# Kernel tuning notes

Hardware: AMD Instinct MI355X
Metric: run time of the kernel (lower is better)

The kernel has to match this reference:

```python
import jax, jax.numpy as jnp
import numpy as np

GRID = 28
P = GRID * GRID  # 784 grid points
BY = 1.0 / 13.5  # grid spacing from DTMWeightWrapperLayer(by=1/13.5)
_c = BY * np.stack(np.meshgrid(np.arange(GRID), np.arange(GRID), indexing='ij'), -1).reshape(P, 2).astype(np.float32)
_D2np = ((_c[:, None, :] - _c[None, :, :]) ** 2).sum(-1)
_ORDERnp = np.argsort(_D2np, axis=1)  # per-grid-point neighbor order (constant)
D2S = jnp.asarray(np.take_along_axis(_D2np, _ORDERnp, axis=1), dtype=jnp.float32)  # [P,P] sorted sq dists
ORDER = jnp.asarray(_ORDERnp, dtype=jnp.int32)
TSEQ_A = jnp.asarray(np.linspace(0.06, 0.3, 25), dtype=jnp.float32); KK_A = (0, 1)
TSEQ_B = jnp.asarray(np.linspace(0.14, 0.4, 27), dtype=jnp.float32); KK_B = (0, 1, 2)

def _conv(x, k):
    return jax.lax.conv_general_dilated(x, k, (1, 1), 'SAME', dimension_numbers=('NHWC', 'HWIO', 'NHWC'))

def _dtm(w, m0):
    # distance-to-measure: w [B,P] nonneg weights on the 28x28 grid -> dtm values [B,P]
    ws = w[:, ORDER]                      # [B,P,P] weights ordered by distance from each grid point
    cum = jnp.cumsum(ws, axis=-1)
    m0W = m0 * jnp.sum(w, axis=-1)[:, None, None]  # mass threshold per sample
    eff = jnp.clip(m0W - (cum - ws), 0.0, ws)      # effective weight used from each neighbor
    return jnp.sqrt(jnp.sum(eff * D2S[None], axis=-1) / m0W[:, :, 0])

def _topo(f, tseq, kk, W, b):
    # persistence-landscape features: lambda_k(t) = k-th largest tent value over grid points
    tmax = tseq[-1]
    tent = jnp.maximum(0.0, jnp.minimum(tseq[None, :, None] - f[:, None, :], (tmax - tseq)[None, :, None]))  # [B,T,P]
    top, _ = jax.lax.top_k(tent, max(kk) + 1)       # [B,T,kmax]
    lam = top[..., jnp.asarray(kk)]                 # [B,T,|KK|]
    return lam.reshape(f.shape[0], -1) @ W + b

def setup_inputs() -> dict:
    key = jax.random.key(0)
    ks = jax.random.split(key, 16)
    r = lambda i, s: (0.05 * jax.random.normal(ks[i], s)).astype(jnp.float32)
    z = lambda n: jnp.zeros((n,), jnp.float32)
    return {
        'x': jax.random.uniform(ks[0], (16, 28, 28, 1), jnp.float32),
        'k11': r(1, (3, 3, 1, 32)), 'cb11': z(32), 'k12': r(2, (3, 3, 32, 1)), 'cb12': z(1),
        'k31': r(3, (3, 3, 1, 32)), 'cb31': z(32), 'k32': r(4, (3, 3, 32, 1)), 'cb32': z(1),
        'k41': r(5, (3, 3, 1, 32)), 'cb41': z(32), 'k42': r(6, (3, 3, 32, 1)), 'cb42': z(1),
        'W33': r(7, (50, 16)), 'b33': z(16), 'W43': r(8, (81, 16)), 'b43': z(16),
        'W5': r(9, (50, 16)), 'b5': z(16), 'W6': r(10, (81, 16)), 'b6': z(16),
        'W7': r(11, (848, 64)), 'b7': z(64), 'W8': r(12, (64, 10)), 'b8': z(10),
    }

def reference(x, k11, cb11, k12, cb12, k31, cb31, k32, cb32, k41, cb41, k42, cb42,
              W33, b33, W43, b43, W5, b5, W6, b6, W7, b7, W8, b8):
    relu = jax.nn.relu
    B = 16
    # CNN branch on raw image
    x1 = relu(_conv(relu(_conv(x, k11) + cb11), k12) + cb12).reshape(B, P)
    # DTM functions on the grid
    x2 = x.reshape(B, P)
    x2_1 = _dtm(x2, 0.05)
    x2_2 = _dtm(x2, 0.2)
    # CNN on DTM(m0=0.05) then topo layer
    x3 = relu(_conv(relu(_conv(x2_1.reshape(B, GRID, GRID, 1), k31) + cb31), k32) + cb32).reshape(B, P)
    x3 = relu(_topo(x3, TSEQ_A, KK_A, W33, b33))
    # CNN on DTM(m0=0.2) then topo layer
    x4 = relu(_conv(relu(_conv(x2_2.reshape(B, GRID, GRID, 1), k41) + cb41), k42) + cb42).reshape(B, P)
    x4 = relu(_topo(x4, TSEQ_B, KK_B, W43, b43))
    # topo layers directly on DTM functions
    x5 = relu(_topo(x2_1, TSEQ_A, KK_A, W5, b5))
    x6 = relu(_topo(x2_2, TSEQ_B, KK_B, W6, b6))
    xc = jnp.concatenate((x1, x3, x4, x5, x6), axis=-1)  # [16,848]
    return relu(xc @ W7 + b7) @ W8 + b8  # [16,10]
```

## Files before the change

kernel.cpp:

```cpp
#include <hip/hip_runtime.h>
#include <math.h>

#define GRID 28
#define NP 784

struct PairTab { unsigned int pk[NP]; float d2[NP]; };
constexpr PairTab make_pairs() {
    PairTab t{};
    int cnt[1459] = {};
    for (int di = 0; di < GRID; ++di)
        for (int dj = 0; dj < GRID; ++dj) cnt[di*di + dj*dj]++;
    int off[1459] = {};
    int acc = 0;
    for (int s = 0; s < 1459; ++s) { off[s] = acc; acc += cnt[s]; }
    const double BY2 = (1.0/13.5) * (1.0/13.5);
    for (int di = 0; di < GRID; ++di)
        for (int dj = 0; dj < GRID; ++dj) {
            int s = di*di + dj*dj;
            int o = off[s]++;
            t.pk[o] = (unsigned)((di << 8) | dj);
            t.d2[o] = (float)((double)s * BY2);
        }
    return t;
}
__constant__ PairTab d_PT = make_pairs();

#define CB_SMEM 7328
__device__ void conv_band(const float* __restrict__ in,
                          const float* __restrict__ kA, const float* __restrict__ cbA,
                          const float* __restrict__ kB, const float* __restrict__ cbB,
                          float* __restrict__ outImg, int r0, float* smem)
{
    float* inl = smem;
    float* kAl = inl + 240;
    float* kBl = kAl + 288;
    float* cbl = kBl + 288;
    float* h   = cbl + 32;
    const int tid = threadIdx.x;
    const float cbB0 = cbB[0];

    if (tid < 288)      { kAl[tid] = kA[tid]; kBl[tid] = kB[tid]; }
    else if (tid < 320) cbl[tid - 288] = cbA[tid - 288];
    else if (tid < 560) {
        const int i = tid - 320;
        const int lr = i / 30, col = i % 30;
        const int y = r0 - 2 + lr, ix = col - 1;
        inl[i] = ((unsigned)y < GRID && (unsigned)ix < GRID) ? in[y*GRID + ix] : 0.f;
    }
    {
        float4* h4 = (float4*)h;
        for (int i = tid; i < 6480/4; i += 1024) h4[i] = make_float4(0.f,0.f,0.f,0.f);
    }
    __syncthreads();

    if (tid < 896) {
        const int c = tid & 31, xx = tid >> 5;
        float ka0 = kAl[0*32+c], ka1 = kAl[1*32+c], ka2 = kAl[2*32+c];
        float ka3 = kAl[3*32+c], ka4 = kAl[4*32+c], ka5 = kAl[5*32+c];
        float ka6 = kAl[6*32+c], ka7 = kAl[7*32+c], ka8 = kAl[8*32+c];
        const float bias = cbl[c];
        float w00 = inl[0*30+xx], w01 = inl[0*30+xx+1], w02 = inl[0*30+xx+2];
        float w10 = inl[1*30+xx], w11 = inl[1*30+xx+1], w12 = inl[1*30+xx+2];
        float w20 = inl[2*30+xx], w21 = inl[2*30+xx+1], w22 = inl[2*30+xx+2];
        #pragma unroll
        for (int s = 0; s < 6; ++s) {
            const int y = r0 - 1 + s;
            float a = bias;
            a = fmaf(w00, ka0, a); a = fmaf(w01, ka1, a); a = fmaf(w02, ka2, a);
            a = fmaf(w10, ka3, a); a = fmaf(w11, ka4, a); a = fmaf(w12, ka5, a);
            a = fmaf(w20, ka6, a); a = fmaf(w21, ka7, a); a = fmaf(w22, ka8, a);
            if ((unsigned)y < GRID) h[(s*30 + xx + 1)*36 + c] = fmaxf(a, 0.f);
            if (s < 5) {
                w00 = w10; w01 = w11; w02 = w12;
                w10 = w20; w11 = w21; w12 = w22;
                w20 = inl[(s+3)*30+xx]; w21 = inl[(s+3)*30+xx+1]; w22 = inl[(s+3)*30+xx+2];
            }
        }
    }
    __syncthreads();

    if (tid < 448) {
        const int part = tid & 3, o = tid >> 2;
        const int xx = o % 28, ly = o / 28;
        const int y = r0 + ly;
        float a = 0.f;
        #pragma unroll
        for (int dy = 0; dy < 3; ++dy) {
            #pragma unroll
            for (int dx = 0; dx < 3; ++dx) {
                const float4* hb = (const float4*)&h[((ly+dy)*30 + xx+dx)*36 + part*8];
                const float4* kb = (const float4*)&kBl[(dy*3+dx)*32 + part*8];
                const float4 h0 = hb[0], h1 = hb[1];
                const float4 k0 = kb[0], k1 = kb[1];
                a += h0.x*k0.x; a += h0.y*k0.y; a += h0.z*k0.z; a += h0.w*k0.w;
                a += h1.x*k1.x; a += h1.y*k1.y; a += h1.z*k1.z; a += h1.w*k1.w;
            }
        }
        a += __shfl_xor(a, 1, 64);
        a += __shfl_xor(a, 2, 64);
        if (part == 0) outImg[y*GRID + xx] = fmaxf(a + cbB0, 0.f);
    }
}

__global__ __launch_bounds__(1024, 8) void k1_kernel(const float* __restrict__ x,
        const float* __restrict__ k11, const float* __restrict__ cb11,
        const float* __restrict__ k12, const float* __restrict__ cb12,
        float* __restrict__ ws)
{
    __shared__ float smem[CB_SMEM];
    const int blk = blockIdx.x;
    const int tid = threadIdx.x;

    if (blk < 112) {
        const int img = blk / 7, band = blk % 7;
        conv_band(x + img*NP, k11, cb11, k12, cb12, ws + 25088 + img*NP, band*4, smem);
        return;
    }

    float* wimg = smem;
    float* red  = smem + 784;
    float* out1 = ws;
    float* out2 = ws + 12544;
    const int dblk = blk - 112;
    const int img = dblk / 49, grp = dblk % 49;
    const int w = tid >> 6, lane = tid & 63;

    float v = 0.f;
    if (tid < NP) { v = x[img*NP + tid]; wimg[tid] = v; }
    for (int off = 32; off; off >>= 1) v += __shfl_down(v, off, 64);
    if (lane == 0) red[w] = v;
    __syncthreads();
    float sumw = 0.f;
    #pragma unroll
    for (int i = 0; i < 16; ++i) sumw += red[i];

    const int pix = grp*16 + w;
    const int pr = pix / GRID, pc = pix % GRID;
    const float m0W1 = 0.05f * sumw;
    const float m0W2 = 0.2f  * sumw;
    float a1 = 0.f, a2 = 0.f, carry = 0.f;

    for (int k0 = 0; k0 < NP; k0 += 64) {
        const int idx = k0 + lane;
        const int ii  = idx < NP ? idx : NP-1;
        const unsigned p = d_PT.pk[ii];
        const float dd   = d_PT.d2[ii];
        const int di = (int)(p >> 8);
        const int dj = (int)(p & 255u);
        const int dG = di * GRID;
        const bool rpOK = (pr + di) < GRID;
        const bool rmOK = pr >= di;
        const bool cpOK = (pc + dj) < GRID;
        const bool cmOK = pc >= dj;
        float Wg = 0.f;
        if (rpOK && cpOK)               Wg += wimg[pix + dG + dj];
        if (dj && rpOK && cmOK)         Wg += wimg[pix + dG - dj];
        if (di && rmOK && cpOK)         Wg += wimg[pix - dG + dj];
        if (di && dj && rmOK && cmOK)   Wg += wimg[pix - dG - dj];
        if (idx >= NP) Wg = 0.f;
        float incl = Wg;
        #pragma unroll
        for (int d = 1; d < 64; d <<= 1) {
            const float t = __shfl_up(incl, d, 64);
            if (lane >= d) incl += t;
        }
        const float cumb = carry + (incl - Wg);
        const float e1 = fminf(fmaxf(m0W1 - cumb, 0.f), Wg);
        const float e2 = fminf(fmaxf(m0W2 - cumb, 0.f), Wg);
        a1 = fmaf(e1, dd, a1);
        a2 = fmaf(e2, dd, a2);
        carry += __shfl(incl, 63, 64);
        if (carry >= m0W2) break;
    }
    for (int m = 32; m; m >>= 1) { a1 += __shfl_xor(a1, m, 64); a2 += __shfl_xor(a2, m, 64); }
    if (lane == 0) {
        out1[img*NP + pix] = sqrtf(a1 / m0W1);
        out2[img*NP + pix] = sqrtf(a2 / m0W2);
    }
}

__global__ __launch_bounds__(1024, 8) void k2_kernel(
        const float* __restrict__ k31, const float* __restrict__ cb31,
        const float* __restrict__ k32, const float* __restrict__ cb32,
        const float* __restrict__ k41, const float* __restrict__ cb41,
        const float* __restrict__ k42, const float* __restrict__ cb42,
        float* __restrict__ ws)
{
    __shared__ float smem[CB_SMEM];
    const int blk = blockIdx.x;
    const float* x2_1 = ws;
    const float* x2_2 = ws + 12544;
    float* x3c = ws + 37632;
    float* x4c = ws + 50176;

    if (blk < 112) {
        const int img = blk / 7, band = blk % 7;
        conv_band(x2_1 + img*NP, k31, cb31, k32, cb32, x3c + img*NP, band*4, smem);
    } else {
        const int c = blk - 112;
        const int img = c / 7, band = c % 7;
        conv_band(x2_2 + img*NP, k41, cb41, k42, cb42, x4c + img*NP, band*4, smem);
    }
}

__device__ __forceinline__ float tseqA(int i) {
    if (i == 24) return 0.3f;
    return (float)((double)i * ((0.3 - 0.06)/24.0) + 0.06);
}
__device__ __forceinline__ float tseqB(int i) {
    if (i == 26) return 0.4f;
    return (float)((double)i * ((0.4 - 0.14)/26.0) + 0.14);
}

__device__ __forceinline__ void merge3(float& m0, float& m1, float& m2,
                                       float b0, float b1, float b2) {
    float r0, r1, r2;
    if (m0 <= b0) {
        r0 = m0;
        if (m1 <= b0) { r1 = m1; r2 = fminf(m2, b0); }
        else          { r1 = b0; r2 = fminf(m1, b1); }
    } else {
        r0 = b0;
        if (b1 <= m0) { r1 = b1; r2 = fminf(b2, m0); }
        else          { r1 = m0; r2 = fminf(m1, b1); }
    }
    m0 = r0; m1 = r1; m2 = r2;
}

__global__ __launch_bounds__(1024) void tail_kernel(
        const float* __restrict__ W33, const float* __restrict__ b33,
        const float* __restrict__ W43, const float* __restrict__ b43,
        const float* __restrict__ W5,  const float* __restrict__ b5,
        const float* __restrict__ W6,  const float* __restrict__ b6,
        const float* __restrict__ W7,  const float* __restrict__ b7,
        const float* __restrict__ W8,  const float* __restrict__ b8,
        const float* __restrict__ ws,  float* __restrict__ out)
{
    __shared__ float xc[848];
    __shared__ float part[1024];
    __shared__ float h7[64];
    __shared__ float fsh[16];
    const int b = blockIdx.x, tid = threadIdx.x;
    const int w = tid >> 6, lane = tid & 63;
    const float* x2_1 = ws;
    const float* x2_2 = ws + 12544;
    const float* x1o  = ws + 25088;
    const float* x3c  = ws + 37632;
    const float* x4c  = ws + 50176;

    if (tid < NP) xc[tid] = x1o[b*NP + tid];

    if (w < 4) {
        const float* src = (w == 0) ? x3c : (w == 1) ? x4c : (w == 2) ? x2_1 : x2_2;
        src += b*NP;
        float m0 = INFINITY, m1 = INFINITY, m2 = INFINITY;
        for (int i = lane; i < NP; i += 64) {
            const float v = src[i];
            if (v < m0)      { m2 = m1; m1 = m0; m0 = v; }
            else if (v < m1) { m2 = m1; m1 = v; }
            else if (v < m2) { m2 = v; }
        }
        for (int mask = 1; mask <= 32; mask <<= 1) {
            const float b0 = __shfl_xor(m0, mask, 64);
            const float b1 = __shfl_xor(m1, mask, 64);
            const float b2 = __shfl_xor(m2, mask, 64);
            merge3(m0, m1, m2, b0, b1, b2);
        }
        if (lane == 0) { fsh[w*3+0] = m0; fsh[w*3+1] = m1; fsh[w*3+2] = m2; }
    }
    __syncthreads();

    if (w < 4) {
        const int g = lane >> 4, j = lane & 15;
        const float f0 = fsh[w*3+0], f1 = fsh[w*3+1], f2 = fsh[w*3+2];
        float acc = 0.f;
        if (w == 0 || w == 2) {
            const float* Wm = (w == 0) ? W33 : W5;
            for (int i = g; i < 50; i += 4) {
                const int t = i >> 1, k = i & 1;
                const float ts = tseqA(t);
                const float fk = k ? f1 : f0;
                const float lam = fmaxf(fminf(ts - fk, 0.3f - ts), 0.f);
                acc = fmaf(lam, Wm[i*16 + j], acc);
            }
        } else {
            const float* Wm = (w == 1) ? W43 : W6;
            for (int i = g; i < 81; i += 4) {
                const int t = i / 3, k = i - t*3;
                const float ts = tseqB(t);
                const float fk = (k == 0) ? f0 : (k == 1 ? f1 : f2);
                const float lam = fmaxf(fminf(ts - fk, 0.4f - ts), 0.f);
                acc = fmaf(lam, Wm[i*16 + j], acc);
            }
        }
        acc += __shfl_xor(acc, 16, 64);
        acc += __shfl_xor(acc, 32, 64);
        if (lane < 16) {
            const float* bv = (w == 0) ? b33 : (w == 1) ? b43 : (w == 2) ? b5 : b6;
            xc[784 + w*16 + lane] = fmaxf(acc + bv[lane], 0.f);
        }
    }
    __syncthreads();

    {
        float acc = 0.f;
        const int i0 = w * 53;
        for (int i = i0; i < i0 + 53; ++i) acc = fmaf(xc[i], W7[i*64 + lane], acc);
        part[w*64 + lane] = acc;
    }
    __syncthreads();
    if (tid < 64) {
        float s = b7[tid];
        #pragma unroll
        for (int k = 0; k < 16; ++k) s += part[k*64 + tid];
        h7[tid] = fmaxf(s, 0.f);
    }
    __syncthreads();

    if (w < 10) {
        float a2 = h7[lane] * W8[lane*10 + w];
        for (int m = 32; m; m >>= 1) a2 += __shfl_down(a2, m, 64);
        if (lane == 0) out[b*10 + w] = a2 + b8[w];
    }
}

extern "C" void kernel_launch(void* const* d_in, const int* in_sizes, int n_in,
                              void* d_out, int out_size, void* d_ws, size_t ws_size,
                              hipStream_t stream)
{
    const float* x    = (const float*)d_in[0];
    const float* k11  = (const float*)d_in[1];
    const float* cb11 = (const float*)d_in[2];
    const float* k12  = (const float*)d_in[3];
    const float* cb12 = (const float*)d_in[4];
    const float* k31  = (const float*)d_in[5];
    const float* cb31 = (const float*)d_in[6];
    const float* k32  = (const float*)d_in[7];
    const float* cb32 = (const float*)d_in[8];
    const float* k41  = (const float*)d_in[9];
    const float* cb41 = (const float*)d_in[10];
    const float* k42  = (const float*)d_in[11];
    const float* cb42 = (const float*)d_in[12];
    const float* W33  = (const float*)d_in[13];
    const float* b33  = (const float*)d_in[14];
    const float* W43  = (const float*)d_in[15];
    const float* b43  = (const float*)d_in[16];
    const float* W5   = (const float*)d_in[17];
    const float* b5   = (const float*)d_in[18];
    const float* W6   = (const float*)d_in[19];
    const float* b6   = (const float*)d_in[20];
    const float* W7   = (const float*)d_in[21];
    const float* b7   = (const float*)d_in[22];
    const float* W8   = (const float*)d_in[23];
    const float* b8   = (const float*)d_in[24];
    float* ws  = (float*)d_ws;
    float* out = (float*)d_out;

    k1_kernel  <<<dim3(896), dim3(1024), 0, stream>>>(x, k11, cb11, k12, cb12, ws);
    k2_kernel  <<<dim3(224), dim3(1024), 0, stream>>>(k31, cb31, k32, cb32,
                                                      k41, cb41, k42, cb42, ws);
    tail_kernel<<<dim3(16),  dim3(1024), 0, stream>>>(W33, b33, W43, b43, W5, b5, W6, b6,
                                                      W7, b7, W8, b8, ws, out);
}
```

Before: 31.36 us.

## Fuse DTM-branch convolutions into tail kernel, one block per image

Removes the separate k2 convolution kernel and performs both 2-layer convolution stacks on the DTM maps inside the tail kernel, with one 1024-thread block per image, in two 14-row halves using shared memory. This eliminates one kernel launch and the global round-trip of the conv outputs. It also unrolls the loops and starts the W7 matvec over the CNN part before the topo features are ready. The cost is that the conv work previously spread over 224 blocks now runs on only 16 blocks, serialised four times per block.

```diff
diff --git a/kernel.cpp b/kernel.cpp
--- a/kernel.cpp
+++ b/kernel.cpp
@@ -179,30 +179,6 @@
     }
 }
 
-__global__ __launch_bounds__(1024, 8) void k2_kernel(
-        const float* __restrict__ k31, const float* __restrict__ cb31,
-        const float* __restrict__ k32, const float* __restrict__ cb32,
-        const float* __restrict__ k41, const float* __restrict__ cb41,
-        const float* __restrict__ k42, const float* __restrict__ cb42,
-        float* __restrict__ ws)
-{
-    __shared__ float smem[CB_SMEM];
-    const int blk = blockIdx.x;
-    const float* x2_1 = ws;
-    const float* x2_2 = ws + 12544;
-    float* x3c = ws + 37632;
-    float* x4c = ws + 50176;
-
-    if (blk < 112) {
-        const int img = blk / 7, band = blk % 7;
-        conv_band(x2_1 + img*NP, k31, cb31, k32, cb32, x3c + img*NP, band*4, smem);
-    } else {
-        const int c = blk - 112;
-        const int img = c / 7, band = c % 7;
-        conv_band(x2_2 + img*NP, k41, cb41, k42, cb42, x4c + img*NP, band*4, smem);
-    }
-}
-
 __device__ __forceinline__ float tseqA(int i) {
     if (i == 24) return 0.3f;
     return (float)((double)i * ((0.3 - 0.06)/24.0) + 0.06);
@@ -227,7 +203,82 @@
     m0 = r0; m1 = r1; m2 = r2;
 }
 
-__global__ __launch_bounds__(1024) void tail_kernel(
+__device__ __forceinline__ void ins3(float& m0, float& m1, float& m2, float v) {
+    if (v < m0)      { m2 = m1; m1 = m0; m0 = v; }
+    else if (v < m1) { m2 = m1; m1 = v; }
+    else if (v < m2) { m2 = v; }
+}
+
+__device__ void conv14(const float* __restrict__ inp,
+                       const float* __restrict__ kA, const float* __restrict__ kB,
+                       const float* __restrict__ cbA, float cbB0,
+                       float* __restrict__ h, float* __restrict__ outL, int r0)
+{
+    const int tid = threadIdx.x;
+    {
+        float4* h4 = (float4*)h;
+        for (int i = tid; i < 17280/4; i += 1024) h4[i] = make_float4(0.f,0.f,0.f,0.f);
+    }
+    __syncthreads();
+
+    if (tid < 896) {
+        const int c = tid & 31, xx = tid >> 5;
+        const float ka0 = kA[0*32+c], ka1 = kA[1*32+c], ka2 = kA[2*32+c];
+        const float ka3 = kA[3*32+c], ka4 = kA[4*32+c], ka5 = kA[5*32+c];
+        const float ka6 = kA[6*32+c], ka7 = kA[7*32+c], ka8 = kA[8*32+c];
+        const float bias = cbA[c];
+        const int y0 = (r0 == 0) ? 0 : r0 - 1;
+        float w00 = inp[y0*30+xx],     w01 = inp[y0*30+xx+1],     w02 = inp[y0*30+xx+2];
+        float w10 = inp[(y0+1)*30+xx], w11 = inp[(y0+1)*30+xx+1], w12 = inp[(y0+1)*30+xx+2];
+        float w20 = inp[(y0+2)*30+xx], w21 = inp[(y0+2)*30+xx+1], w22 = inp[(y0+2)*30+xx+2];
+        #pragma unroll
+        for (int s = 0; s < 15; ++s) {
+            const int y = y0 + s;
+            float a = bias;
+            a = fmaf(w00, ka0, a); a = fmaf(w01, ka1, a); a = fmaf(w02, ka2, a);
+            a = fmaf(w10, ka3, a); a = fmaf(w11, ka4, a); a = fmaf(w12, ka5, a);
+            a = fmaf(w20, ka6, a); a = fmaf(w21, ka7, a); a = fmaf(w22, ka8, a);
+            const int lr = y - (r0 - 1);
+            h[(lr*30 + xx + 1)*36 + c] = fmaxf(a, 0.f);
+            if (s < 14) {
+                w00 = w10; w01 = w11; w02 = w12;
+                w10 = w20; w11 = w21; w12 = w22;
+                const int py = y0 + s + 3;
+                w20 = inp[py*30+xx]; w21 = inp[py*30+xx+1]; w22 = inp[py*30+xx+2];
+            }
+        }
+    }
+    __syncthreads();
+
+    for (int t = tid; t < 1568; t += 1024) {
+        const int part = t & 3, o = t >> 2;
+        const int xx = o % 28, ly = o / 28;
+        const int y = r0 + ly;
+        float a = 0.f;
+        #pragma unroll
+        for (int dy = 0; dy < 3; ++dy) {
+            #pragma unroll
+            for (int dx = 0; dx < 3; ++dx) {
+                const float4* hb = (const float4*)&h[((ly+dy)*30 + xx+dx)*36 + part*8];
+                const float4* kb = (const float4*)&kB[(dy*3+dx)*32 + part*8];
+                const float4 h0 = hb[0], h1 = hb[1];
+                const float4 k0 = kb[0], k1 = kb[1];
+                a += h0.x*k0.x; a += h0.y*k0.y; a += h0.z*k0.z; a += h0.w*k0.w;
+                a += h1.x*k1.x; a += h1.y*k1.y; a += h1.z*k1.z; a += h1.w*k1.w;
+            }
+        }
+        a += __shfl_xor(a, 1, 64);
+        a += __shfl_xor(a, 2, 64);
+        if (part == 0) outL[y*GRID + xx] = fmaxf(a + cbB0, 0.f);
+    }
+    __syncthreads();
+}
+
+__global__ __launch_bounds__(1024) void fused_kernel(
+        const float* __restrict__ k31, const float* __restrict__ cb31,
+        const float* __restrict__ k32, const float* __restrict__ cb32,
+        const float* __restrict__ k41, const float* __restrict__ cb41,
+        const float* __restrict__ k42, const float* __restrict__ cb42,
         const float* __restrict__ W33, const float* __restrict__ b33,
         const float* __restrict__ W43, const float* __restrict__ b43,
         const float* __restrict__ W5,  const float* __restrict__ b5,
@@ -236,29 +287,60 @@
         const float* __restrict__ W8,  const float* __restrict__ b8,
         const float* __restrict__ ws,  float* __restrict__ out)
 {
-    __shared__ float xc[848];
-    __shared__ float part[1024];
-    __shared__ float h7[64];
-    __shared__ float fsh[16];
+    __shared__ float smem[23808];
+    float* h    = smem;
+    float* xc   = smem + 17280;
+    float* in1p = smem + 18128;
+    float* in2p = smem + 19028;
+    float* x3o  = smem + 19928;
+    float* x4o  = smem + 20712;
+    float* kw   = smem + 21496;
+    float* cba  = smem + 22648;
+    float* cbb2 = smem + 22712;
+    float* part = smem + 22714;
+    float* h7f  = smem + 23738;
+
     const int b = blockIdx.x, tid = threadIdx.x;
     const int w = tid >> 6, lane = tid & 63;
     const float* x2_1 = ws;
     const float* x2_2 = ws + 12544;
     const float* x1o  = ws + 25088;
-    const float* x3c  = ws + 37632;
-    const float* x4c  = ws + 50176;
 
     if (tid < NP) xc[tid] = x1o[b*NP + tid];
+    if (tid < 900) {
+        const int r = tid / 30, c = tid % 30;
+        const bool in_ = (r >= 1 && r <= 28 && c >= 1 && c <= 28);
+        const int gi = b*NP + (r-1)*GRID + (c-1);
+        in1p[tid] = in_ ? x2_1[gi] : 0.f;
+        in2p[tid] = in_ ? x2_2[gi] : 0.f;
+    }
+    for (int i = tid; i < 1152; i += 1024) {
+        kw[i] = (i < 288) ? k31[i] : (i < 576) ? k32[i-288]
+              : (i < 864) ? k41[i-576] : k42[i-864];
+    }
+    if (tid < 64) cba[tid] = (tid < 32) ? cb31[tid] : cb41[tid-32];
+    if (tid < 2)  cbb2[tid] = (tid == 0) ? cb32[0] : cb42[0];
+    __syncthreads();
+
+    conv14(in1p, kw,       kw+288, cba,      cbb2[0], h, x3o, 0);
+    conv14(in1p, kw,       kw+288, cba,      cbb2[0], h, x3o, 14);
+    conv14(in2p, kw+576,   kw+864, cba+32,   cbb2[1], h, x4o, 0);
+    conv14(in2p, kw+576,   kw+864, cba+32,   cbb2[1], h, x4o, 14);
+
+    float acc = 0.f;
+    const float* Wp = W7 + lane;
+    const int i0 = w * 53;
 
     if (w < 4) {
-        const float* src = (w == 0) ? x3c : (w == 1) ? x4c : (w == 2) ? x2_1 : x2_2;
-        src += b*NP;
+        const float* srcG = (w == 2) ? (x2_1 + b*NP) : (x2_2 + b*NP);
+        const float* srcL = (w == 0) ? x3o : x4o;
         float m0 = INFINITY, m1 = INFINITY, m2 = INFINITY;
-        for (int i = lane; i < NP; i += 64) {
-            const float v = src[i];
-            if (v < m0)      { m2 = m1; m1 = m0; m0 = v; }
-            else if (v < m1) { m2 = m1; m1 = v; }
-            else if (v < m2) { m2 = v; }
+        #pragma unroll
+        for (int k = 0; k < 13; ++k) {
+            const int i = k*64 + lane;
+            float v = INFINITY;
+            if (i < NP) v = (w < 2) ? srcL[i] : srcG[i];
+            ins3(m0, m1, m2, v);
         }
         for (int mask = 1; mask <= 32; mask <<= 1) {
             const float b0 = __shfl_xor(m0, mask, 64);
@@ -266,59 +348,70 @@
             const float b2 = __shfl_xor(m2, mask, 64);
             merge3(m0, m1, m2, b0, b1, b2);
         }
-        if (lane == 0) { fsh[w*3+0] = m0; fsh[w*3+1] = m1; fsh[w*3+2] = m2; }
-    }
-    __syncthreads();
-
-    if (w < 4) {
+        const float f0 = m0, f1 = m1, f2 = m2;
+
         const int g = lane >> 4, j = lane & 15;
-        const float f0 = fsh[w*3+0], f1 = fsh[w*3+1], f2 = fsh[w*3+2];
-        float acc = 0.f;
+        float at = 0.f;
         if (w == 0 || w == 2) {
             const float* Wm = (w == 0) ? W33 : W5;
-            for (int i = g; i < 50; i += 4) {
-                const int t = i >> 1, k = i & 1;
-                const float ts = tseqA(t);
-                const float fk = k ? f1 : f0;
-                const float lam = fmaxf(fminf(ts - fk, 0.3f - ts), 0.f);
-                acc = fmaf(lam, Wm[i*16 + j], acc);
+            #pragma unroll
+            for (int r = 0; r < 13; ++r) {
+                const int i = g + 4*r;
+                if (i < 50) {
+                    const int t = i >> 1, k = i & 1;
+                    const float ts = tseqA(t);
+                    const float fk = k ? f1 : f0;
+                    const float lam = fmaxf(fminf(ts - fk, 0.3f - ts), 0.f);
+                    at = fmaf(lam, Wm[i*16 + j], at);
+                }
             }
         } else {
             const float* Wm = (w == 1) ? W43 : W6;
-            for (int i = g; i < 81; i += 4) {
-                const int t = i / 3, k = i - t*3;
-                const float ts = tseqB(t);
-                const float fk = (k == 0) ? f0 : (k == 1 ? f1 : f2);
-                const float lam = fmaxf(fminf(ts - fk, 0.4f - ts), 0.f);
-                acc = fmaf(lam, Wm[i*16 + j], acc);
-            }
-        }
-        acc += __shfl_xor(acc, 16, 64);
-        acc += __shfl_xor(acc, 32, 64);
+            #pragma unroll
+            for (int r = 0; r < 21; ++r) {
+                const int i = g + 4*r;
+                if (i < 81) {
+                    const int t = i / 3, k = i - t*3;
+                    const float ts = tseqB(t);
+                    const float fk = (k == 0) ? f0 : (k == 1 ? f1 : f2);
+                    const float lam = fmaxf(fminf(ts - fk, 0.4f - ts), 0.f);
+                    at = fmaf(lam, Wm[i*16 + j], at);
+                }
+            }
+        }
+        at += __shfl_xor(at, 16, 64);
+        at += __shfl_xor(at, 32, 64);
         if (lane < 16) {
             const float* bv = (w == 0) ? b33 : (w == 1) ? b43 : (w == 2) ? b5 : b6;
-            xc[784 + w*16 + lane] = fmaxf(acc + bv[lane], 0.f);
-        }
-    }
-    __syncthreads();
-
-    {
-        float acc = 0.f;
-        const int i0 = w * 53;
-        for (int i = i0; i < i0 + 53; ++i) acc = fmaf(xc[i], W7[i*64 + lane], acc);
-        part[w*64 + lane] = acc;
-    }
-    __syncthreads();
+            xc[784 + w*16 + lane] = fmaxf(at + bv[lane], 0.f);
+        }
+    }
+
+    #pragma unroll
+    for (int r = 0; r < 53; ++r) {
+        const int i = i0 + r;
+        if (i < NP) acc = fmaf(xc[i], Wp[i*64], acc);
+    }
+    __syncthreads();
+
+    #pragma unroll
+    for (int r = 0; r < 53; ++r) {
+        const int i = i0 + r;
+        if (i >= NP) acc = fmaf(xc[i], Wp[i*64], acc);
+    }
+    part[w*64 + lane] = acc;
+    __syncthreads();
+
     if (tid < 64) {
         float s = b7[tid];
         #pragma unroll
         for (int k = 0; k < 16; ++k) s += part[k*64 + tid];
-        h7[tid] = fmaxf(s, 0.f);
+        h7f[tid] = fmaxf(s, 0.f);
     }
     __syncthreads();
 
     if (w < 10) {
-        float a2 = h7[lane] * W8[lane*10 + w];
+        float a2 = h7f[lane] * W8[lane*10 + w];
         for (int m = 32; m; m >>= 1) a2 += __shfl_down(a2, m, 64);
         if (lane == 0) out[b*10 + w] = a2 + b8[w];
     }
@@ -356,9 +449,9 @@
     float* ws  = (float*)d_ws;
     float* out = (float*)d_out;
 
-    k1_kernel  <<<dim3(896), dim3(1024), 0, stream>>>(x, k11, cb11, k12, cb12, ws);
-    k2_kernel  <<<dim3(224), dim3(1024), 0, stream>>>(k31, cb31, k32, cb32,
-                                                      k41, cb41, k42, cb42, ws);
-    tail_kernel<<<dim3(16),  dim3(1024), 0, stream>>>(W33, b33, W43, b43, W5, b5, W6, b6,
-                                                      W7, b7, W8, b8, ws, out);
-}
+    k1_kernel   <<<dim3(896), dim3(1024), 0, stream>>>(x, k11, cb11, k12, cb12, ws);
+    fused_kernel<<<dim3(16),  dim3(1024), 0, stream>>>(k31, cb31, k32, cb32,
+                                                       k41, cb41, k42, cb42,
+                                                       W33, b33, W43, b43, W5, b5,
+                                                       W6, b6, W7, b7, W8, b8, ws, out);
+}
```

After: 57.99 us. +84.9%, slower.

## Move bottom-3 reductions and DTM topo layers into conv kernel, shrink tail

Applied to the files above, without the earlier changes.

The conv kernel now computes per-band bottom-3 minima of its outputs and writes them to workspace. It also runs 32 extra blocks that do the min-3 reduction and topo layer for the two DTM maps. The tail kernel then only merges seven small triplets per branch instead of scanning four 784-element arrays serially, which shortens the serial single-block critical path. The cost is an extra sync and shared buffer in conv blocks, plus unrolled W7 loads in the tail.

```diff
diff --git a/kernel.cpp b/kernel.cpp
--- a/kernel.cpp
+++ b/kernel.cpp
@@ -25,17 +25,40 @@
 }
 __constant__ PairTab d_PT = make_pairs();
 
-#define CB_SMEM 7328
+__device__ __forceinline__ void merge3(float& m0, float& m1, float& m2,
+                                       float b0, float b1, float b2) {
+    float r0, r1, r2;
+    if (m0 <= b0) {
+        r0 = m0;
+        if (m1 <= b0) { r1 = m1; r2 = fminf(m2, b0); }
+        else          { r1 = b0; r2 = fminf(m1, b1); }
+    } else {
+        r0 = b0;
+        if (b1 <= m0) { r1 = b1; r2 = fminf(b2, m0); }
+        else          { r1 = m0; r2 = fminf(m1, b1); }
+    }
+    m0 = r0; m1 = r1; m2 = r2;
+}
+
+__device__ __forceinline__ void ins3(float& m0, float& m1, float& m2, float v) {
+    if (v < m0)      { m2 = m1; m1 = m0; m0 = v; }
+    else if (v < m1) { m2 = m1; m1 = v; }
+    else if (v < m2) { m2 = v; }
+}
+
+#define CB_SMEM 7440
 __device__ void conv_band(const float* __restrict__ in,
                           const float* __restrict__ kA, const float* __restrict__ cbA,
                           const float* __restrict__ kB, const float* __restrict__ cbB,
-                          float* __restrict__ outImg, int r0, float* smem)
+                          float* __restrict__ outImg, int r0, float* smem,
+                          float* __restrict__ minTrip)
 {
-    float* inl = smem;
-    float* kAl = inl + 240;
-    float* kBl = kAl + 288;
-    float* cbl = kBl + 288;
-    float* h   = cbl + 32;
+    float* inl   = smem;
+    float* kAl   = inl + 240;
+    float* kBl   = kAl + 288;
+    float* cbl   = kBl + 288;
+    float* h     = cbl + 32;
+    float* outSm = h + 6480;
     const int tid = threadIdx.x;
     const float cbB0 = cbB[0];
 
@@ -98,7 +121,27 @@
         }
         a += __shfl_xor(a, 1, 64);
         a += __shfl_xor(a, 2, 64);
-        if (part == 0) outImg[y*GRID + xx] = fmaxf(a + cbB0, 0.f);
+        if (part == 0) {
+            const float v = fmaxf(a + cbB0, 0.f);
+            outImg[y*GRID + xx] = v;
+            if (minTrip) outSm[o] = v;
+        }
+    }
+
+    if (minTrip) {
+        __syncthreads();
+        if (tid < 64) {
+            float m0 = INFINITY, m1 = INFINITY, m2 = INFINITY;
+            ins3(m0, m1, m2, outSm[tid]);
+            if (tid < 48) ins3(m0, m1, m2, outSm[64 + tid]);
+            for (int mask = 1; mask <= 32; mask <<= 1) {
+                const float b0 = __shfl_xor(m0, mask, 64);
+                const float b1 = __shfl_xor(m1, mask, 64);
+                const float b2 = __shfl_xor(m2, mask, 64);
+                merge3(m0, m1, m2, b0, b1, b2);
+            }
+            if (tid == 0) { minTrip[0] = m0; minTrip[1] = m1; minTrip[2] = m2; }
+        }
     }
 }
 
@@ -113,7 +156,8 @@
 
     if (blk < 112) {
         const int img = blk / 7, band = blk % 7;
-        conv_band(x + img*NP, k11, cb11, k12, cb12, ws + 25088 + img*NP, band*4, smem);
+        conv_band(x + img*NP, k11, cb11, k12, cb12, ws + 25088 + img*NP, band*4, smem,
+                  (float*)0);
         return;
     }
 
@@ -179,125 +223,146 @@
     }
 }
 
+__device__ __forceinline__ float tseqA(int i) {
+    if (i == 24) return 0.3f;
+    return (float)((double)i * ((0.3 - 0.06)/24.0) + 0.06);
+}
+__device__ __forceinline__ float tseqB(int i) {
+    if (i == 26) return 0.4f;
+    return (float)((double)i * ((0.4 - 0.14)/26.0) + 0.14);
+}
+
+__device__ __forceinline__ float topoA_partial(const float* __restrict__ Wm,
+                                               float f0, float f1, int lane) {
+    const int g = lane >> 4, j = lane & 15;
+    float at = 0.f;
+    #pragma unroll
+    for (int r = 0; r < 13; ++r) {
+        const int i = g + 4*r;
+        if (i < 50) {
+            const int t = i >> 1, k = i & 1;
+            const float ts = tseqA(t);
+            const float fk = k ? f1 : f0;
+            const float lam = fmaxf(fminf(ts - fk, 0.3f - ts), 0.f);
+            at = fmaf(lam, Wm[i*16 + j], at);
+        }
+    }
+    return at;
+}
+__device__ __forceinline__ float topoB_partial(const float* __restrict__ Wm,
+                                               float f0, float f1, float f2, int lane) {
+    const int g = lane >> 4, j = lane & 15;
+    float at = 0.f;
+    #pragma unroll
+    for (int r = 0; r < 21; ++r) {
+        const int i = g + 4*r;
+        if (i < 81) {
+            const int t = i / 3, k = i - t*3;
+            const float ts = tseqB(t);
+            const float fk = (k == 0) ? f0 : (k == 1 ? f1 : f2);
+            const float lam = fmaxf(fminf(ts - fk, 0.4f - ts), 0.f);
+            at = fmaf(lam, Wm[i*16 + j], at);
+        }
+    }
+    return at;
+}
+
 __global__ __launch_bounds__(1024, 8) void k2_kernel(
         const float* __restrict__ k31, const float* __restrict__ cb31,
         const float* __restrict__ k32, const float* __restrict__ cb32,
         const float* __restrict__ k41, const float* __restrict__ cb41,
         const float* __restrict__ k42, const float* __restrict__ cb42,
+        const float* __restrict__ W5,  const float* __restrict__ b5,
+        const float* __restrict__ W6,  const float* __restrict__ b6,
         float* __restrict__ ws)
 {
     __shared__ float smem[CB_SMEM];
     const int blk = blockIdx.x;
+    const int tid = threadIdx.x;
     const float* x2_1 = ws;
     const float* x2_2 = ws + 12544;
-    float* x3c = ws + 37632;
-    float* x4c = ws + 50176;
+    float* x3c   = ws + 37632;
+    float* x4c   = ws + 50176;
+    float* trip3 = ws + 62720;
+    float* trip4 = ws + 63056;
+    float* topo5 = ws + 63392;
+    float* topo6 = ws + 63648;
 
     if (blk < 112) {
         const int img = blk / 7, band = blk % 7;
-        conv_band(x2_1 + img*NP, k31, cb31, k32, cb32, x3c + img*NP, band*4, smem);
-    } else {
+        conv_band(x2_1 + img*NP, k31, cb31, k32, cb32, x3c + img*NP, band*4, smem,
+                  trip3 + (img*7 + band)*3);
+    } else if (blk < 224) {
         const int c = blk - 112;
         const int img = c / 7, band = c % 7;
-        conv_band(x2_2 + img*NP, k41, cb41, k42, cb42, x4c + img*NP, band*4, smem);
-    }
-}
-
-__device__ __forceinline__ float tseqA(int i) {
-    if (i == 24) return 0.3f;
-    return (float)((double)i * ((0.3 - 0.06)/24.0) + 0.06);
-}
-__device__ __forceinline__ float tseqB(int i) {
-    if (i == 26) return 0.4f;
-    return (float)((double)i * ((0.4 - 0.14)/26.0) + 0.14);
-}
-
-__device__ __forceinline__ void merge3(float& m0, float& m1, float& m2,
-                                       float b0, float b1, float b2) {
-    float r0, r1, r2;
-    if (m0 <= b0) {
-        r0 = m0;
-        if (m1 <= b0) { r1 = m1; r2 = fminf(m2, b0); }
-        else          { r1 = b0; r2 = fminf(m1, b1); }
+        conv_band(x2_2 + img*NP, k41, cb41, k42, cb42, x4c + img*NP, band*4, smem,
+                  trip4 + (img*7 + band)*3);
     } else {
-        r0 = b0;
-        if (b1 <= m0) { r1 = b1; r2 = fminf(b2, m0); }
-        else          { r1 = m0; r2 = fminf(m1, b1); }
-    }
-    m0 = r0; m1 = r1; m2 = r2;
+        if (tid >= 64) return;
+        const int idx = blk - 224;
+        const int arr = idx >> 4, img = idx & 15;
+        const float* src = (arr == 0) ? (x2_1 + img*NP) : (x2_2 + img*NP);
+        const int lane = tid;
+        float m0 = INFINITY, m1 = INFINITY, m2 = INFINITY;
+        #pragma unroll
+        for (int k = 0; k < 13; ++k) {
+            const int i = k*64 + lane;
+            const float v = (i < NP) ? src[i] : INFINITY;
+            ins3(m0, m1, m2, v);
+        }
+        for (int mask = 1; mask <= 32; mask <<= 1) {
+            const float b0 = __shfl_xor(m0, mask, 64);
+            const float b1 = __shfl_xor(m1, mask, 64);
+            const float b2 = __shfl_xor(m2, mask, 64);
+            merge3(m0, m1, m2, b0, b1, b2);
+        }
+        float at = (arr == 0) ? topoA_partial(W5, m0, m1, lane)
+                              : topoB_partial(W6, m0, m1, m2, lane);
+        at += __shfl_xor(at, 16, 64);
+        at += __shfl_xor(at, 32, 64);
+        if (lane < 16) {
+            const float* bv = (arr == 0) ? b5 : b6;
+            float* dst = (arr == 0) ? topo5 : topo6;
+            dst[img*16 + lane] = fmaxf(at + bv[lane], 0.f);
+        }
+    }
 }
 
 __global__ __launch_bounds__(1024) void tail_kernel(
         const float* __restrict__ W33, const float* __restrict__ b33,
         const float* __restrict__ W43, const float* __restrict__ b43,
-        const float* __restrict__ W5,  const float* __restrict__ b5,
-        const float* __restrict__ W6,  const float* __restrict__ b6,
         const float* __restrict__ W7,  const float* __restrict__ b7,
         const float* __restrict__ W8,  const float* __restrict__ b8,
         const float* __restrict__ ws,  float* __restrict__ out)
 {
     __shared__ float xc[848];
     __shared__ float part[1024];
-    __shared__ float h7[64];
-    __shared__ float fsh[16];
+    __shared__ float h7f[64];
     const int b = blockIdx.x, tid = threadIdx.x;
     const int w = tid >> 6, lane = tid & 63;
-    const float* x2_1 = ws;
-    const float* x2_2 = ws + 12544;
-    const float* x1o  = ws + 25088;
-    const float* x3c  = ws + 37632;
-    const float* x4c  = ws + 50176;
+    const float* x1o   = ws + 25088;
+    const float* trip3 = ws + 62720;
+    const float* trip4 = ws + 63056;
+    const float* topo5 = ws + 63392;
+    const float* topo6 = ws + 63648;
 
     if (tid < NP) xc[tid] = x1o[b*NP + tid];
-
-    if (w < 4) {
-        const float* src = (w == 0) ? x3c : (w == 1) ? x4c : (w == 2) ? x2_1 : x2_2;
-        src += b*NP;
-        float m0 = INFINITY, m1 = INFINITY, m2 = INFINITY;
-        for (int i = lane; i < NP; i += 64) {
-            const float v = src[i];
-            if (v < m0)      { m2 = m1; m1 = m0; m0 = v; }
-            else if (v < m1) { m2 = m1; m1 = v; }
-            else if (v < m2) { m2 = v; }
-        }
-        for (int mask = 1; mask <= 32; mask <<= 1) {
-            const float b0 = __shfl_xor(m0, mask, 64);
-            const float b1 = __shfl_xor(m1, mask, 64);
-            const float b2 = __shfl_xor(m2, mask, 64);
-            merge3(m0, m1, m2, b0, b1, b2);
-        }
-        if (lane == 0) { fsh[w*3+0] = m0; fsh[w*3+1] = m1; fsh[w*3+2] = m2; }
-    }
-    __syncthreads();
-
-    if (w < 4) {
-        const int g = lane >> 4, j = lane & 15;
-        const float f0 = fsh[w*3+0], f1 = fsh[w*3+1], f2 = fsh[w*3+2];
-        float acc = 0.f;
-        if (w == 0 || w == 2) {
-            const float* Wm = (w == 0) ? W33 : W5;
-            for (int i = g; i < 50; i += 4) {
-                const int t = i >> 1, k = i & 1;
-                const float ts = tseqA(t);
-                const float fk = k ? f1 : f0;
-                const float lam = fmaxf(fminf(ts - fk, 0.3f - ts), 0.f);
-                acc = fmaf(lam, Wm[i*16 + j], acc);
-            }
-        } else {
-            const float* Wm = (w == 1) ? W43 : W6;
-            for (int i = g; i < 81; i += 4) {
-                const int t = i / 3, k = i - t*3;
-                const float ts = tseqB(t);
-                const float fk = (k == 0) ? f0 : (k == 1 ? f1 : f2);
-                const float lam = fmaxf(fminf(ts - fk, 0.4f - ts), 0.f);
-                acc = fmaf(lam, Wm[i*16 + j], acc);
-            }
-        }
-        acc += __shfl_xor(acc, 16, 64);
-        acc += __shfl_xor(acc, 32, 64);
+    if (w == 2 && lane < 16) xc[816 + lane] = topo5[b*16 + lane];
+    if (w == 3 && lane < 16) xc[832 + lane] = topo6[b*16 + lane];
+
+    if (w < 2) {
+        const float* tp = ((w == 0) ? trip3 : trip4) + b*21;
+        float m0 = tp[0], m1 = tp[1], m2 = tp[2];
+        #pragma unroll
+        for (int s = 1; s < 7; ++s)
+            merge3(m0, m1, m2, tp[s*3], tp[s*3+1], tp[s*3+2]);
+        float at = (w == 0) ? topoA_partial(W33, m0, m1, lane)
+                            : topoB_partial(W43, m0, m1, m2, lane);
+        at += __shfl_xor(at, 16, 64);
+        at += __shfl_xor(at, 32, 64);
         if (lane < 16) {
-            const float* bv = (w == 0) ? b33 : (w == 1) ? b43 : (w == 2) ? b5 : b6;
-            xc[784 + w*16 + lane] = fmaxf(acc + bv[lane], 0.f);
+            const float* bv = (w == 0) ? b33 : b43;
+            xc[784 + w*16 + lane] = fmaxf(at + bv[lane], 0.f);
         }
     }
     __syncthreads();
@@ -305,7 +370,10 @@
     {
         float acc = 0.f;
         const int i0 = w * 53;
-        for (int i = i0; i < i0 + 53; ++i) acc = fmaf(xc[i], W7[i*64 + lane], acc);
+        const float* Wp = W7 + i0*64 + lane;
+        #pragma unroll
+        for (int r = 0; r < 53; ++r)
+            acc = fmaf(xc[i0 + r], Wp[r*64], acc);
         part[w*64 + lane] = acc;
     }
     __syncthreads();
@@ -313,12 +381,12 @@
         float s = b7[tid];
         #pragma unroll
         for (int k = 0; k < 16; ++k) s += part[k*64 + tid];
-        h7[tid] = fmaxf(s, 0.f);
+        h7f[tid] = fmaxf(s, 0.f);
     }
     __syncthreads();
 
     if (w < 10) {
-        float a2 = h7[lane] * W8[lane*10 + w];
+        float a2 = h7f[lane] * W8[lane*10 + w];
         for (int m = 32; m; m >>= 1) a2 += __shfl_down(a2, m, 64);
         if (lane == 0) out[b*10 + w] = a2 + b8[w];
     }
@@ -357,8 +425,9 @@
     float* out = (float*)d_out;
 
     k1_kernel  <<<dim3(896), dim3(1024), 0, stream>>>(x, k11, cb11, k12, cb12, ws);
-    k2_kernel  <<<dim3(224), dim3(1024), 0, stream>>>(k31, cb31, k32, cb32,
-                                                      k41, cb41, k42, cb42, ws);
-    tail_kernel<<<dim3(16),  dim3(1024), 0, stream>>>(W33, b33, W43, b43, W5, b5, W6, b6,
+    k2_kernel  <<<dim3(256), dim3(1024), 0, stream>>>(k31, cb31, k32, cb32,
+                                                      k41, cb41, k42, cb42,
+                                                      W5, b5, W6, b6, ws);
+    tail_kernel<<<dim3(16),  dim3(1024), 0, stream>>>(W33, b33, W43, b43,
                                                       W7, b7, W8, b8, ws, out);
 }
```

New measurement: 30.20 us. 3.7% less time.
